# Kernel tuning notes

Measured on AMD Instinct MI355X. Metric: run time of the kernel, lower is better.

The kernel has to match this reference:

```python
import jax, jax.numpy as jnp
import numpy as np

N = 8192
D = 256

def setup_inputs() -> dict:
    key = jax.random.key(0)
    k1, k2, k3 = jax.random.split(key, 3)
    x = jax.random.normal(k1, (N, D), dtype=jnp.float32)
    adj_t = jax.random.uniform(k2, (N, N), dtype=jnp.float32)
    adj_t2 = jax.random.uniform(k3, (N, N), dtype=jnp.float32)
    return {"x": x, "adj_t": adj_t, "adj_t2": adj_t2}

def reference(x, adj_t, adj_t2):
    # H2GCN neighborhood aggregation: 1-hop and 2-hop adjacency matmuls, concat on feature dim.
    x1 = adj_t @ x    # [N, D]
    x2 = adj_t2 @ x   # [N, D]
    return jnp.concatenate([x1, x2], axis=1)  # [N, 2D]
```

## Files before the change

### kernel.cpp

```cpp
#include <hip/hip_runtime.h>
#include <stdint.h>
#include <stddef.h>

#define N_TOT  8192
#define D_FEAT 256
#define BM 32
#define BK 64
#define LDK 72
#define K_ITERS (N_TOT / BK)

typedef float f32x4_t __attribute__((ext_vector_type(4)));
typedef short s16x8_t __attribute__((ext_vector_type(8)));

__device__ __forceinline__ unsigned short f2bf(float f) {
    union { float f; unsigned int u; } a;
    a.f = f;
    unsigned int r = a.u + 0x7FFFu + ((a.u >> 16) & 1u);
    return (unsigned short)(r >> 16);
}

__device__ __forceinline__ f32x4_t ldg_nt(const float* p) {
    return __builtin_nontemporal_load((const f32x4_t*)p);
}

__global__ __launch_bounds__(256) void xpose_kernel(
    const float* __restrict__ x, unsigned short* __restrict__ xT)
{
    __shared__ unsigned short T[64 * 72];
    const int t  = threadIdx.x;
    const int k0 = blockIdx.x * 64;
    const int n0 = blockIdx.y * 64;

    #pragma unroll
    for (int i = 0; i < 4; ++i) {
        const int kr = (t >> 4) + 16 * i;
        const int c4 = (t & 15) * 4;
        float4 v = *(const float4*)(x + (size_t)(k0 + kr) * D_FEAT + n0 + c4);
        T[(c4 + 0) * 72 + kr] = f2bf(v.x);
        T[(c4 + 1) * 72 + kr] = f2bf(v.y);
        T[(c4 + 2) * 72 + kr] = f2bf(v.z);
        T[(c4 + 3) * 72 + kr] = f2bf(v.w);
    }
    __syncthreads();
    #pragma unroll
    for (int i = 0; i < 2; ++i) {
        const int n  = (t >> 3) + 32 * i;
        const int c8 = (t & 7) * 8;
        uint4 w = *(const uint4*)&T[n * 72 + c8];
        *(uint4*)(xT + (size_t)(n0 + n) * N_TOT + k0 + c8) = w;
    }
}

__global__ __launch_bounds__(512, 4) void h2gcn_kernel(
    const float* __restrict__ adj0,
    const float* __restrict__ adj1,
    const unsigned short* __restrict__ xT,
    float* __restrict__ out)
{
    const int g  = blockIdx.y;
    const float* __restrict__ adj = g ? adj1 : adj0;
    const int m0   = blockIdx.x * BM;
    const int t    = threadIdx.x;
    const int lane = t & 63;
    const int w    = t >> 6;
    const int fl   = lane & 15;
    const int fq   = lane >> 4;

    __shared__ __align__(16) unsigned short Asm[2][BM * LDK];

    const int a_row = t >> 4;
    const int a_c4  = (t & 15) * 4;
    const float* aBase = adj + (size_t)(m0 + a_row) * N_TOT + a_c4;

    const unsigned short* bBase0 = xT + (size_t)(32 * w + fl) * N_TOT + 8 * fq;
    const unsigned short* bBase1 = bBase0 + (size_t)16 * N_TOT;

    f32x4_t aR[2];
    s16x8_t bR[2][2][2];
    f32x4_t acc[2][2];

    #pragma unroll
    for (int mt = 0; mt < 2; ++mt)
        #pragma unroll
        for (int nt = 0; nt < 2; ++nt) {
            f32x4_t z = {0.0f, 0.0f, 0.0f, 0.0f};
            acc[mt][nt] = z;
        }

    f32x4_t a0 = ldg_nt(aBase);
    aR[1]      = ldg_nt(aBase + BK);
    aR[0]      = ldg_nt(aBase + 2 * BK);
    #pragma unroll
    for (int ks = 0; ks < 2; ++ks) {
        bR[0][0][ks] = *(const s16x8_t*)(bBase0 + 32 * ks);
        bR[0][1][ks] = *(const s16x8_t*)(bBase1 + 32 * ks);
    }
    {
        ushort4 v;
        v.x = f2bf(a0.x); v.y = f2bf(a0.y);
        v.z = f2bf(a0.z); v.w = f2bf(a0.w);
        *(ushort4*)&Asm[0][a_row * LDK + a_c4] = v;
    }
    __syncthreads();

    #pragma unroll 2
    for (int it = 0; it < K_ITERS; ++it) {
        const int cur = it & 1;
        const int nxt = cur ^ 1;

        {
            ushort4 v;
            v.x = f2bf(aR[nxt].x); v.y = f2bf(aR[nxt].y);
            v.z = f2bf(aR[nxt].z); v.w = f2bf(aR[nxt].w);
            *(ushort4*)&Asm[nxt][a_row * LDK + a_c4] = v;
        }

        s16x8_t af[2][2];
        #pragma unroll
        for (int mt = 0; mt < 2; ++mt)
            #pragma unroll
            for (int ks = 0; ks < 2; ++ks)
                af[mt][ks] = *(const s16x8_t*)&Asm[cur][(16 * mt + fl) * LDK + 32 * ks + 8 * fq];

        const int ta = (it + 3 < K_ITERS) ? (it + 3) : (K_ITERS - 1);
        const int tb = (it + 1 < K_ITERS) ? (it + 1) : (K_ITERS - 1);
        const size_t ka = (size_t)ta * BK;
        const size_t kb = (size_t)tb * BK;
        aR[nxt] = ldg_nt(aBase + ka);
        #pragma unroll
        for (int ks = 0; ks < 2; ++ks) {
            bR[nxt][0][ks] = *(const s16x8_t*)(bBase0 + kb + 32 * ks);
            bR[nxt][1][ks] = *(const s16x8_t*)(bBase1 + kb + 32 * ks);
        }

        asm volatile("s_waitcnt lgkmcnt(0)" ::: "memory");
        __builtin_amdgcn_sched_barrier(0);
        __builtin_amdgcn_s_barrier();

        #pragma unroll
        for (int ks = 0; ks < 2; ++ks)
            #pragma unroll
            for (int mt = 0; mt < 2; ++mt)
                #pragma unroll
                for (int nt = 0; nt < 2; ++nt)
                    acc[mt][nt] = __builtin_amdgcn_mfma_f32_16x16x32_bf16(
                        af[mt][ks], bR[cur][nt][ks], acc[mt][nt], 0, 0, 0);
    }

    #pragma unroll
    for (int mt = 0; mt < 2; ++mt)
        #pragma unroll
        for (int nt = 0; nt < 2; ++nt)
            #pragma unroll
            for (int r = 0; r < 4; ++r) {
                const int row = m0 + 16 * mt + 4 * fq + r;
                const int col = g * D_FEAT + 32 * w + 16 * nt + fl;
                out[(size_t)row * (2 * D_FEAT) + col] = acc[mt][nt][r];
            }
}

extern "C" void kernel_launch(void* const* d_in, const int* in_sizes, int n_in,
                              void* d_out, int out_size, void* d_ws, size_t ws_size,
                              hipStream_t stream) {
    const float* x      = (const float*)d_in[0];
    const float* adj_t  = (const float*)d_in[1];
    const float* adj_t2 = (const float*)d_in[2];
    float* out = (float*)d_out;
    unsigned short* xT = (unsigned short*)d_ws;
    (void)in_sizes; (void)n_in; (void)out_size; (void)ws_size;

    hipLaunchKernelGGL(xpose_kernel, dim3(N_TOT / 64, D_FEAT / 64), dim3(256), 0, stream, x, xT);
    hipLaunchKernelGGL(h2gcn_kernel, dim3(N_TOT / BM, 2), dim3(512), 0, stream,
                       adj_t, adj_t2, xT, out);
}
```

Baseline: 658.7 us.

## Fuse both adjacency matmuls per block to share x tiles, swizzle LDS layout

Each block now handles the same 32 rows of both adjacency matrices, so every xT B-fragment loaded from global memory feeds two sets of accumulators. The grid's second dimension is dropped and occupancy is lowered to 2 blocks per SM. A-tile loads widen to 8 floats per thread and are written to an XOR-swizzled fragment-major LDS layout to avoid bank conflicts. Output stores become nontemporal. The cost is more registers per thread and fewer resident blocks.

```diff
diff --git a/kernel.cpp b/kernel.cpp
--- a/kernel.cpp
+++ b/kernel.cpp
@@ -6,7 +6,6 @@
 #define D_FEAT 256
 #define BM 32
 #define BK 64
-#define LDK 72
 #define K_ITERS (N_TOT / BK)
 
 typedef float f32x4_t __attribute__((ext_vector_type(4)));
@@ -19,8 +18,12 @@
     return (unsigned short)(r >> 16);
 }
 
-__device__ __forceinline__ f32x4_t ldg_nt(const float* p) {
-    return __builtin_nontemporal_load((const f32x4_t*)p);
+struct f32x8 { f32x4_t lo, hi; };
+__device__ __forceinline__ f32x8 ld8_nt(const float* p) {
+    f32x8 v;
+    v.lo = __builtin_nontemporal_load((const f32x4_t*)p);
+    v.hi = __builtin_nontemporal_load((const f32x4_t*)(p + 4));
+    return v;
 }
 
 __global__ __launch_bounds__(256) void xpose_kernel(
@@ -51,14 +54,12 @@
     }
 }
 
-__global__ __launch_bounds__(512, 4) void h2gcn_kernel(
+__global__ __launch_bounds__(512, 2) void h2gcn_kernel(
     const float* __restrict__ adj0,
     const float* __restrict__ adj1,
     const unsigned short* __restrict__ xT,
     float* __restrict__ out)
 {
-    const int g  = blockIdx.y;
-    const float* __restrict__ adj = g ? adj1 : adj0;
     const int m0   = blockIdx.x * BM;
     const int t    = threadIdx.x;
     const int lane = t & 63;
@@ -66,40 +67,50 @@
     const int fl   = lane & 15;
     const int fq   = lane >> 4;
 
-    __shared__ __align__(16) unsigned short Asm[2][BM * LDK];
+    __shared__ __align__(16) unsigned short Asm[2][512 * 8];
 
-    const int a_row = t >> 4;
-    const int a_c4  = (t & 15) * 4;
-    const float* aBase = adj + (size_t)(m0 + a_row) * N_TOT + a_c4;
+    const int gsel = t >> 8;
+    const int r_l  = ((t >> 6) & 3) * 8 + ((t >> 3) & 7);
+    const int c_w  = t & 7;
+    const int ks_w = c_w >> 2, fq_w = c_w & 3;
+    const int mt_w = r_l >> 4,  fl_w = r_l & 15;
+    const int wslot = ((gsel * 2 + mt_w) * 2 + ks_w) * 64 + fq_w * 16
+                    + ((fl_w ^ (4 * ks_w + fq_w)) & 15);
+    const float* aBase = (gsel ? adj1 : adj0)
+                       + (size_t)(m0 + r_l) * N_TOT + c_w * 8;
 
     const unsigned short* bBase0 = xT + (size_t)(32 * w + fl) * N_TOT + 8 * fq;
     const unsigned short* bBase1 = bBase0 + (size_t)16 * N_TOT;
 
-    f32x4_t aR[2];
+    f32x8   aR[2];
     s16x8_t bR[2][2][2];
-    f32x4_t acc[2][2];
+    f32x4_t acc[2][2][2];
 
     #pragma unroll
-    for (int mt = 0; mt < 2; ++mt)
+    for (int g = 0; g < 2; ++g)
         #pragma unroll
-        for (int nt = 0; nt < 2; ++nt) {
-            f32x4_t z = {0.0f, 0.0f, 0.0f, 0.0f};
-            acc[mt][nt] = z;
-        }
+        for (int mt = 0; mt < 2; ++mt)
+            #pragma unroll
+            for (int nt = 0; nt < 2; ++nt) {
+                f32x4_t z = {0.0f, 0.0f, 0.0f, 0.0f};
+                acc[g][mt][nt] = z;
+            }
 
-    f32x4_t a0 = ldg_nt(aBase);
-    aR[1]      = ldg_nt(aBase + BK);
-    aR[0]      = ldg_nt(aBase + 2 * BK);
+    f32x8 a0 = ld8_nt(aBase);
+    aR[1]    = ld8_nt(aBase + BK);
+    aR[0]    = ld8_nt(aBase + 2 * BK);
     #pragma unroll
     for (int ks = 0; ks < 2; ++ks) {
         bR[0][0][ks] = *(const s16x8_t*)(bBase0 + 32 * ks);
         bR[0][1][ks] = *(const s16x8_t*)(bBase1 + 32 * ks);
     }
     {
-        ushort4 v;
-        v.x = f2bf(a0.x); v.y = f2bf(a0.y);
-        v.z = f2bf(a0.z); v.w = f2bf(a0.w);
-        *(ushort4*)&Asm[0][a_row * LDK + a_c4] = v;
+        s16x8_t pk;
+        pk[0] = (short)f2bf(a0.lo.x); pk[1] = (short)f2bf(a0.lo.y);
+        pk[2] = (short)f2bf(a0.lo.z); pk[3] = (short)f2bf(a0.lo.w);
+        pk[4] = (short)f2bf(a0.hi.x); pk[5] = (short)f2bf(a0.hi.y);
+        pk[6] = (short)f2bf(a0.hi.z); pk[7] = (short)f2bf(a0.hi.w);
+        *(s16x8_t*)&Asm[0][wslot * 8] = pk;
     }
     __syncthreads();
 
@@ -109,24 +120,30 @@
         const int nxt = cur ^ 1;
 
         {
-            ushort4 v;
-            v.x = f2bf(aR[nxt].x); v.y = f2bf(aR[nxt].y);
-            v.z = f2bf(aR[nxt].z); v.w = f2bf(aR[nxt].w);
-            *(ushort4*)&Asm[nxt][a_row * LDK + a_c4] = v;
+            s16x8_t pk;
+            pk[0] = (short)f2bf(aR[nxt].lo.x); pk[1] = (short)f2bf(aR[nxt].lo.y);
+            pk[2] = (short)f2bf(aR[nxt].lo.z); pk[3] = (short)f2bf(aR[nxt].lo.w);
+            pk[4] = (short)f2bf(aR[nxt].hi.x); pk[5] = (short)f2bf(aR[nxt].hi.y);
+            pk[6] = (short)f2bf(aR[nxt].hi.z); pk[7] = (short)f2bf(aR[nxt].hi.w);
+            *(s16x8_t*)&Asm[nxt][wslot * 8] = pk;
         }
 
-        s16x8_t af[2][2];
+        s16x8_t af[2][2][2];
         #pragma unroll
-        for (int mt = 0; mt < 2; ++mt)
+        for (int g = 0; g < 2; ++g)
             #pragma unroll
-            for (int ks = 0; ks < 2; ++ks)
-                af[mt][ks] = *(const s16x8_t*)&Asm[cur][(16 * mt + fl) * LDK + 32 * ks + 8 * fq];
+            for (int mt = 0; mt < 2; ++mt)
+                #pragma unroll
+                for (int ks = 0; ks < 2; ++ks) {
+                    const int slot = ((g * 2 + mt) * 2 + ks) * 64 + fq * 16
+                                   + ((fl ^ (4 * ks + fq)) & 15);
+                    af[g][mt][ks] = *(const s16x8_t*)&Asm[cur][slot * 8];
+                }
 
         const int ta = (it + 3 < K_ITERS) ? (it + 3) : (K_ITERS - 1);
         const int tb = (it + 1 < K_ITERS) ? (it + 1) : (K_ITERS - 1);
-        const size_t ka = (size_t)ta * BK;
+        aR[nxt] = ld8_nt(aBase + (size_t)ta * BK);
         const size_t kb = (size_t)tb * BK;
-        aR[nxt] = ldg_nt(aBase + ka);
         #pragma unroll
         for (int ks = 0; ks < 2; ++ks) {
             bR[nxt][0][ks] = *(const s16x8_t*)(bBase0 + kb + 32 * ks);
@@ -140,23 +157,28 @@
         #pragma unroll
         for (int ks = 0; ks < 2; ++ks)
             #pragma unroll
-            for (int mt = 0; mt < 2; ++mt)
+            for (int g = 0; g < 2; ++g)
                 #pragma unroll
-                for (int nt = 0; nt < 2; ++nt)
-                    acc[mt][nt] = __builtin_amdgcn_mfma_f32_16x16x32_bf16(
-                        af[mt][ks], bR[cur][nt][ks], acc[mt][nt], 0, 0, 0);
+                for (int mt = 0; mt < 2; ++mt)
+                    #pragma unroll
+                    for (int nt = 0; nt < 2; ++nt)
+                        acc[g][mt][nt] = __builtin_amdgcn_mfma_f32_16x16x32_bf16(
+                            af[g][mt][ks], bR[cur][nt][ks], acc[g][mt][nt], 0, 0, 0);
     }
 
     #pragma unroll
-    for (int mt = 0; mt < 2; ++mt)
+    for (int g = 0; g < 2; ++g)
         #pragma unroll
-        for (int nt = 0; nt < 2; ++nt)
+        for (int mt = 0; mt < 2; ++mt)
             #pragma unroll
-            for (int r = 0; r < 4; ++r) {
-                const int row = m0 + 16 * mt + 4 * fq + r;
-                const int col = g * D_FEAT + 32 * w + 16 * nt + fl;
-                out[(size_t)row * (2 * D_FEAT) + col] = acc[mt][nt][r];
-            }
+            for (int nt = 0; nt < 2; ++nt)
+                #pragma unroll
+                for (int r = 0; r < 4; ++r) {
+                    const int row = m0 + 16 * mt + 4 * fq + r;
+                    const int col = g * D_FEAT + 32 * w + 16 * nt + fl;
+                    __builtin_nontemporal_store(acc[g][mt][nt][r],
+                        &out[(size_t)row * (2 * D_FEAT) + col]);
+                }
 }
 
 extern "C" void kernel_launch(void* const* d_in, const int* in_sizes, int n_in,
@@ -170,6 +192,6 @@
     (void)in_sizes; (void)n_in; (void)out_size; (void)ws_size;
 
     hipLaunchKernelGGL(xpose_kernel, dim3(N_TOT / 64, D_FEAT / 64), dim3(256), 0, stream, x, xT);
-    hipLaunchKernelGGL(h2gcn_kernel, dim3(N_TOT / BM, 2), dim3(512), 0, stream,
+    hipLaunchKernelGGL(h2gcn_kernel, dim3(N_TOT / BM), dim3(512), 0, stream,
                        adj_t, adj_t2, xT, out);
 }
```

Result: faster. 569.6 us (-13.5%).

## Process both adjacency matrices per block so each xT tile serves two products

Applied to the files above, without the earlier changes.

Each block now covers 16 rows of both adj_t and adj_t2 rather than 32 rows of one matrix, so every xT fragment loaded into registers feeds MFMAs for both 1-hop and 2-hop outputs. The grid drops to one dimension with twice the blocks along M. The intent is to halve the xT re-reads per output. The LDS A tile uses a new XOR-swizzled slot layout in place of padded rows to avoid bank conflicts, and output stores become nontemporal. The per-block adj traffic is unchanged, and the more complex index math adds some ALU work.

```diff
diff --git a/kernel.cpp b/kernel.cpp
--- a/kernel.cpp
+++ b/kernel.cpp
@@ -4,13 +4,13 @@
 
 #define N_TOT  8192
 #define D_FEAT 256
-#define BM 32
+#define BM 16
 #define BK 64
-#define LDK 72
 #define K_ITERS (N_TOT / BK)
 
 typedef float f32x4_t __attribute__((ext_vector_type(4)));
 typedef short s16x8_t __attribute__((ext_vector_type(8)));
+typedef short s16x4_t __attribute__((ext_vector_type(4)));
 
 __device__ __forceinline__ unsigned short f2bf(float f) {
     union { float f; unsigned int u; } a;
@@ -19,7 +19,7 @@
     return (unsigned short)(r >> 16);
 }
 
-__device__ __forceinline__ f32x4_t ldg_nt(const float* p) {
+__device__ __forceinline__ f32x4_t ld4_nt(const float* p) {
     return __builtin_nontemporal_load((const f32x4_t*)p);
 }
 
@@ -57,8 +57,6 @@
     const unsigned short* __restrict__ xT,
     float* __restrict__ out)
 {
-    const int g  = blockIdx.y;
-    const float* __restrict__ adj = g ? adj1 : adj0;
     const int m0   = blockIdx.x * BM;
     const int t    = threadIdx.x;
     const int lane = t & 63;
@@ -66,11 +64,17 @@
     const int fl   = lane & 15;
     const int fq   = lane >> 4;
 
-    __shared__ __align__(16) unsigned short Asm[2][BM * LDK];
+    __shared__ __align__(16) unsigned short Asm[2][256 * 8];
 
-    const int a_row = t >> 4;
-    const int a_c4  = (t & 15) * 4;
-    const float* aBase = adj + (size_t)(m0 + a_row) * N_TOT + a_c4;
+    const int u   = t >> 1;
+    const int hg  = t & 1;
+    const int sr  = u >> 4;
+    const int sg  = (u >> 3) & 1;
+    const int c8  = u & 7;
+    const int wslot = ((sg * 2 + (c8 >> 2)) * 4 + (c8 & 3)) * 16 + (sr ^ c8);
+    const int woff  = wslot * 8 + hg * 4;
+    const float* aBase = (sg ? adj1 : adj0)
+                       + (size_t)(m0 + sr) * N_TOT + c8 * 8 + hg * 4;
 
     const unsigned short* bBase0 = xT + (size_t)(32 * w + fl) * N_TOT + 8 * fq;
     const unsigned short* bBase1 = bBase0 + (size_t)16 * N_TOT;
@@ -80,26 +84,26 @@
     f32x4_t acc[2][2];
 
     #pragma unroll
-    for (int mt = 0; mt < 2; ++mt)
+    for (int g = 0; g < 2; ++g)
         #pragma unroll
         for (int nt = 0; nt < 2; ++nt) {
             f32x4_t z = {0.0f, 0.0f, 0.0f, 0.0f};
-            acc[mt][nt] = z;
+            acc[g][nt] = z;
         }
 
-    f32x4_t a0 = ldg_nt(aBase);
-    aR[1]      = ldg_nt(aBase + BK);
-    aR[0]      = ldg_nt(aBase + 2 * BK);
+    f32x4_t a0 = ld4_nt(aBase);
+    aR[1]      = ld4_nt(aBase + BK);
+    aR[0]      = ld4_nt(aBase + 2 * BK);
     #pragma unroll
     for (int ks = 0; ks < 2; ++ks) {
         bR[0][0][ks] = *(const s16x8_t*)(bBase0 + 32 * ks);
         bR[0][1][ks] = *(const s16x8_t*)(bBase1 + 32 * ks);
     }
     {
-        ushort4 v;
-        v.x = f2bf(a0.x); v.y = f2bf(a0.y);
-        v.z = f2bf(a0.z); v.w = f2bf(a0.w);
-        *(ushort4*)&Asm[0][a_row * LDK + a_c4] = v;
+        s16x4_t pk;
+        pk[0] = (short)f2bf(a0.x); pk[1] = (short)f2bf(a0.y);
+        pk[2] = (short)f2bf(a0.z); pk[3] = (short)f2bf(a0.w);
+        *(s16x4_t*)&Asm[0][woff] = pk;
     }
     __syncthreads();
 
@@ -109,24 +113,26 @@
         const int nxt = cur ^ 1;
 
         {
-            ushort4 v;
-            v.x = f2bf(aR[nxt].x); v.y = f2bf(aR[nxt].y);
-            v.z = f2bf(aR[nxt].z); v.w = f2bf(aR[nxt].w);
-            *(ushort4*)&Asm[nxt][a_row * LDK + a_c4] = v;
+            s16x4_t pk;
+            pk[0] = (short)f2bf(aR[nxt].x); pk[1] = (short)f2bf(aR[nxt].y);
+            pk[2] = (short)f2bf(aR[nxt].z); pk[3] = (short)f2bf(aR[nxt].w);
+            *(s16x4_t*)&Asm[nxt][woff] = pk;
         }
 
         s16x8_t af[2][2];
         #pragma unroll
-        for (int mt = 0; mt < 2; ++mt)
+        for (int g = 0; g < 2; ++g)
             #pragma unroll
-            for (int ks = 0; ks < 2; ++ks)
-                af[mt][ks] = *(const s16x8_t*)&Asm[cur][(16 * mt + fl) * LDK + 32 * ks + 8 * fq];
+            for (int ks = 0; ks < 2; ++ks) {
+                const int slot = ((g * 2 + ks) * 4 + fq) * 16
+                               + ((fl ^ (4 * ks + fq)) & 15);
+                af[g][ks] = *(const s16x8_t*)&Asm[cur][slot * 8];
+            }
 
         const int ta = (it + 3 < K_ITERS) ? (it + 3) : (K_ITERS - 1);
         const int tb = (it + 1 < K_ITERS) ? (it + 1) : (K_ITERS - 1);
-        const size_t ka = (size_t)ta * BK;
+        aR[nxt] = ld4_nt(aBase + (size_t)ta * BK);
         const size_t kb = (size_t)tb * BK;
-        aR[nxt] = ldg_nt(aBase + ka);
         #pragma unroll
         for (int ks = 0; ks < 2; ++ks) {
             bR[nxt][0][ks] = *(const s16x8_t*)(bBase0 + kb + 32 * ks);
@@ -140,22 +146,23 @@
         #pragma unroll
         for (int ks = 0; ks < 2; ++ks)
             #pragma unroll
-            for (int mt = 0; mt < 2; ++mt)
+            for (int g = 0; g < 2; ++g)
                 #pragma unroll
                 for (int nt = 0; nt < 2; ++nt)
-                    acc[mt][nt] = __builtin_amdgcn_mfma_f32_16x16x32_bf16(
-                        af[mt][ks], bR[cur][nt][ks], acc[mt][nt], 0, 0, 0);
+                    acc[g][nt] = __builtin_amdgcn_mfma_f32_16x16x32_bf16(
+                        af[g][ks], bR[cur][nt][ks], acc[g][nt], 0, 0, 0);
     }
 
     #pragma unroll
-    for (int mt = 0; mt < 2; ++mt)
+    for (int g = 0; g < 2; ++g)
         #pragma unroll
         for (int nt = 0; nt < 2; ++nt)
             #pragma unroll
             for (int r = 0; r < 4; ++r) {
-                const int row = m0 + 16 * mt + 4 * fq + r;
+                const int row = m0 + 4 * fq + r;
                 const int col = g * D_FEAT + 32 * w + 16 * nt + fl;
-                out[(size_t)row * (2 * D_FEAT) + col] = acc[mt][nt][r];
+                __builtin_nontemporal_store(acc[g][nt][r],
+                    &out[(size_t)row * (2 * D_FEAT) + col]);
             }
 }
 
@@ -170,6 +177,6 @@
     (void)in_sizes; (void)n_in; (void)out_size; (void)ws_size;
 
     hipLaunchKernelGGL(xpose_kernel, dim3(N_TOT / 64, D_FEAT / 64), dim3(256), 0, stream, x, xT);
-    hipLaunchKernelGGL(h2gcn_kernel, dim3(N_TOT / BM, 2), dim3(512), 0, stream,
+    hipLaunchKernelGGL(h2gcn_kernel, dim3(N_TOT / BM), dim3(512), 0, stream,
                        adj_t, adj_t2, xT, out);
 }
```

Result: no change. 656.8 us (-0.3%).
